# Optimization experiments

Measured on AMD Instinct MI355X. Metric: run time of the kernel, lower is better.

The kernel has to match this reference:

```python
import jax, jax.numpy as jnp
import numpy as np

N = 2048   # query length
M = 2048   # key length
B = 2      # batch
D = 1024   # model dim (d_x_q = d_x_kv = d_out)
H = 16     # heads
DQK = D // H
DV = D // H
OFFSET = 0


def setup_inputs() -> dict:
    key = jax.random.key(0)
    k1, k2, k3, k4, k5, k6 = jax.random.split(key, 6)
    return {
        "x_q": jax.random.normal(k1, (N, B, D), dtype=jnp.float32),
        "x_kv": jax.random.normal(k2, (M, B, D), dtype=jnp.float32),
        "to_q": jax.random.normal(k3, (H, DQK, D), dtype=jnp.float32),
        "to_kv": jax.random.normal(k4, (H, DQK + DV, D), dtype=jnp.float32),
        "for_pos_enc": jax.random.normal(k5, (H, DQK, D), dtype=jnp.float32),
        "to_o": jax.random.normal(k6, (D, H, DV), dtype=jnp.float32),
    }


def _pos_enc(for_pos_enc, n, m, offset, d_x_kv):
    # relative distances i - j + offset, range [offset-(m-1), offset+(n-1)]
    dmin = offset - (m - 1)
    dmax = offset + (n - 1)
    r = jnp.arange(dmin, dmax + 1, dtype=jnp.float32)            # [R]
    inv_freq = 1.0 / (10000.0 ** (jnp.arange(0.0, d_x_kv, 2.0, dtype=jnp.float32) / d_x_kv))
    phases = r[:, None] * inv_freq[None, :]                       # [R, d/2]
    sincos = jnp.concatenate([jnp.sin(phases), jnp.cos(phases)], axis=-1)  # [R, d]
    table = jnp.einsum('hdb,rb->rhd', for_pos_enc, sincos)       # [R, H, DQK]
    dists = jnp.arange(n)[:, None] - jnp.arange(m)[None, :] + offset
    return table[dists - dmin]                                    # [n, m, H, DQK]


def reference(x_q, x_kv, to_q, to_kv, for_pos_enc, to_o):
    d_qk = to_q.shape[1]
    q = jnp.einsum('hdb,nzb->nzhd', to_q, x_q)     # [N,B,H,DQK]
    kv = jnp.einsum('hdb,mzb->mzhd', to_kv, x_kv)  # [M,B,H,DQK+DV]
    k = kv[..., :d_qk]
    v = kv[..., d_qk:]
    n, m = x_q.shape[0], x_kv.shape[0]

    pos_enc = _pos_enc(for_pos_enc, n, m, OFFSET, x_kv.shape[-1])

    content_logits = jnp.einsum('nzhd,mzhd->nmzh', q, k)          # [N,M,B,H]
    position_logits = jnp.einsum('nzhd,nmhd->nmzh', q, pos_enc)   # [N,M,B,H]
    logits = content_logits + position_logits

    # causal mask: True above diagonal shifted by 1+offset
    mask = jnp.triu(jnp.ones((n, m), dtype=bool), 1 + OFFSET)
    logits = jnp.where(mask[:, :, None, None], -jnp.inf, logits)

    weights = jax.nn.softmax(logits, axis=1)
    attn = jnp.einsum('nmzh,mzhd->nzhd', weights, v)              # [N,B,H,DV]
    out = jnp.einsum('dhb,nzhb->nzd', to_o, attn)                 # [N,B,D]
    return out
```

## Files before the change

### kernel.cpp

```cpp
#include <hip/hip_runtime.h>
#include <math.h>

#define NQ 2048
#define MKV 2048
#define BZ 2
#define DM 1024
#define NH 16
#define DH 64
#define RTAB 4095
#define R0TAB 1984
#define MTAB (RTAB - R0TAB)

typedef __bf16 bf16x8 __attribute__((ext_vector_type(8)));
typedef float f32x4 __attribute__((ext_vector_type(4)));

__device__ inline unsigned short f2bf(float x) {
  union { float f; unsigned u; } v; v.f = x;
  unsigned r = (v.u + 0x7FFFu + ((v.u >> 16) & 1u)) >> 16;
  return (unsigned short)r;
}
__device__ inline float bf2f(unsigned short h) {
  union { unsigned u; float f; } v; v.u = ((unsigned)h) << 16; return v.f;
}

#define SWZ(r, b) ((b) ^ (((r) & 7) << 4))
#define VSWZ(dv, m) \
  ((dv) * 128 + (((((m) >> 3) ^ ((dv) & 7) ^ (((dv) >> 3) & 7)) << 4)) + ((m) & 7) * 2)

__device__ inline void gload_lds16(const void* g, void* l) {
  __builtin_amdgcn_global_load_lds((const __attribute__((address_space(1))) void*)g,
                                   (__attribute__((address_space(3))) void*)l, 16, 0, 0);
}

__global__ __launch_bounds__(256) void prep_kernel(
    const float* __restrict__ i0, unsigned short* __restrict__ h0, unsigned short* __restrict__ l0, int n0,
    const float* __restrict__ i1, unsigned short* __restrict__ h1, unsigned short* __restrict__ l1, int n1,
    const float* __restrict__ i2, unsigned short* __restrict__ h2, unsigned short* __restrict__ l2, int n2,
    const float* __restrict__ i3, unsigned short* __restrict__ h3, unsigned short* __restrict__ l3, int n3,
    const float* __restrict__ i4, unsigned short* __restrict__ h4, unsigned short* __restrict__ l4, int n4_,
    const float* __restrict__ i5, unsigned short* __restrict__ h5, unsigned short* __restrict__ l5, int n5,
    unsigned short* __restrict__ schi, unsigned short* __restrict__ sclo) {
  if (blockIdx.y == 6) {
    for (int idx = blockIdx.x * 256 + threadIdx.x; idx < MTAB * DM; idx += gridDim.x * 256) {
      int r = idx / DM;
      int b = idx - r * DM;
      int i = (b < DM / 2) ? b : (b - DM / 2);
      double fr = exp((double)i * (-9.210340371976184 / 512.0));
      float rr = (float)(R0TAB + r - (MKV - 1));
      float ph = rr * (float)fr;
      float val = (b < DM / 2) ? sinf(ph) : cosf(ph);
      unsigned short hb = f2bf(val);
      schi[idx] = hb;
      sclo[idx] = f2bf(val - bf2f(hb));
    }
    return;
  }
  const float* in; unsigned short* hp; unsigned short* lp; int n4;
  switch (blockIdx.y) {
    case 0: in = i0; hp = h0; lp = l0; n4 = n0; break;
    case 1: in = i1; hp = h1; lp = l1; n4 = n1; break;
    case 2: in = i2; hp = h2; lp = l2; n4 = n2; break;
    case 3: in = i3; hp = h3; lp = l3; n4 = n3; break;
    case 4: in = i4; hp = h4; lp = l4; n4 = n4_; break;
    default: in = i5; hp = h5; lp = l5; n4 = n5; break;
  }
  for (int i = blockIdx.x * 256 + threadIdx.x; i < n4; i += gridDim.x * 256) {
    float4 v = ((const float4*)in)[i];
    float f[4] = {v.x, v.y, v.z, v.w};
    ushort4 hq, lq;
    unsigned short* hh = (unsigned short*)&hq;
    unsigned short* ll = (unsigned short*)&lq;
#pragma unroll
    for (int e = 0; e < 4; ++e) {
      unsigned short hb = f2bf(f[e]);
      hh[e] = hb;
      ll[e] = f2bf(f[e] - bf2f(hb));
    }
    ((ushort4*)hp)[i] = hq;
    ((ushort4*)lp)[i] = lq;
  }
}

template <int SPLIT_OUT>
__device__ __forceinline__ void gemm_body(
    const unsigned short* __restrict__ Ahi, const unsigned short* __restrict__ Alo,
    const unsigned short* __restrict__ Bhi, const unsigned short* __restrict__ Blo,
    float* __restrict__ Cf, unsigned short* __restrict__ Chi, unsigned short* __restrict__ Clo,
    int M, int N, int row0, int col0, char* lds) {
  const int K = 1024;
  char* sAh = lds;
  char* sAl = lds + 16384;
  char* sBh = lds + 32768;
  char* sBl = lds + 49152;
  const int t = threadIdx.x;
  const int w = t >> 6;
  const int lane = t & 63;
  const int lo = lane & 15;
  const int hi = lane >> 4;
  const int wm = w >> 1, wn = w & 1;

  f32x4 acc[4][4];
#pragma unroll
  for (int a = 0; a < 4; ++a)
#pragma unroll
    for (int b = 0; b < 4; ++b) acc[a][b] = (f32x4){0.f, 0.f, 0.f, 0.f};

  for (int k0 = 0; k0 < K; k0 += 64) {
#pragma unroll
    for (int i = 0; i < 4; ++i) {
      int L = i * 4096 + t * 16;
      int r = L >> 7;
      int c16 = (L >> 4) & 7;
      int g16 = c16 ^ (r & 7);
      int ra = row0 + r;
      if (ra >= M) ra = M - 1;
      int rb = col0 + r;
      const char* gah = (const char*)(Ahi + (size_t)ra * K + k0) + g16 * 16;
      const char* gal = (const char*)(Alo + (size_t)ra * K + k0) + g16 * 16;
      const char* gbh = (const char*)(Bhi + (size_t)rb * K + k0) + g16 * 16;
      const char* gbl = (const char*)(Blo + (size_t)rb * K + k0) + g16 * 16;
      gload_lds16(gah, sAh + L);
      gload_lds16(gal, sAl + L);
      gload_lds16(gbh, sBh + L);
      gload_lds16(gbl, sBl + L);
    }
    __syncthreads();
#pragma unroll
    for (int ks = 0; ks < 2; ++ks) {
      bf16x8 ah[4], al[4], bh[4], bl[4];
#pragma unroll
      for (int f = 0; f < 4; ++f) {
        int rA = wm * 64 + 16 * f + lo;
        int offA = rA * 128 + (((4 * ks + hi) ^ (rA & 7)) << 4);
        ah[f] = *(const bf16x8*)(sAh + offA);
        al[f] = *(const bf16x8*)(sAl + offA);
        int rB = wn * 64 + 16 * f + lo;
        int offB = rB * 128 + (((4 * ks + hi) ^ (rB & 7)) << 4);
        bh[f] = *(const bf16x8*)(sBh + offB);
        bl[f] = *(const bf16x8*)(sBl + offB);
      }
#pragma unroll
      for (int fm = 0; fm < 4; ++fm)
#pragma unroll
        for (int fn = 0; fn < 4; ++fn) {
          acc[fm][fn] = __builtin_amdgcn_mfma_f32_16x16x32_bf16(ah[fm], bh[fn], acc[fm][fn], 0, 0, 0);
          acc[fm][fn] = __builtin_amdgcn_mfma_f32_16x16x32_bf16(ah[fm], bl[fn], acc[fm][fn], 0, 0, 0);
          acc[fm][fn] = __builtin_amdgcn_mfma_f32_16x16x32_bf16(al[fm], bh[fn], acc[fm][fn], 0, 0, 0);
        }
    }
    __syncthreads();
  }
#pragma unroll
  for (int fm = 0; fm < 4; ++fm)
#pragma unroll
    for (int qq = 0; qq < 4; ++qq) {
      int row = row0 + wm * 64 + 16 * fm + 4 * hi + qq;
      if (row < M) {
#pragma unroll
        for (int fn = 0; fn < 4; ++fn) {
          int col = col0 + wn * 64 + 16 * fn + lo;
          float v = acc[fm][fn][qq];
          if (SPLIT_OUT) {
            unsigned short hb = f2bf(v);
            Chi[(size_t)row * N + col] = hb;
            Clo[(size_t)row * N + col] = f2bf(v - bf2f(hb));
          } else {
            Cf[(size_t)row * N + col] = v;
          }
        }
      }
    }
}

__global__ __launch_bounds__(256, 2) void gemm3_kernel(
    const unsigned short* __restrict__ xqh, const unsigned short* __restrict__ xql,
    const unsigned short* __restrict__ tqh, const unsigned short* __restrict__ tql,
    unsigned short* __restrict__ qh, unsigned short* __restrict__ ql,
    const unsigned short* __restrict__ xkh, const unsigned short* __restrict__ xkl,
    const unsigned short* __restrict__ tkh, const unsigned short* __restrict__ tkl,
    unsigned short* __restrict__ kvh, unsigned short* __restrict__ kvl,
    const unsigned short* __restrict__ sch, const unsigned short* __restrict__ scl,
    const unsigned short* __restrict__ fph, const unsigned short* __restrict__ fpl,
    unsigned short* __restrict__ tbh, unsigned short* __restrict__ tbl) {
  __shared__ char lds[65536];
  int bx = blockIdx.x;
  if (bx < 256) {
    int gx = bx & 7, gy = bx >> 3;
    gemm_body<1>(xqh, xql, tqh, tql, nullptr, qh, ql, 4096, 1024, gy * 128, gx * 128, lds);
  } else if (bx < 768) {
    bx -= 256;
    int gx = bx & 15, gy = bx >> 4;
    gemm_body<1>(xkh, xkl, tkh, tkl, nullptr, kvh, kvl, 4096, 2048, gy * 128, gx * 128, lds);
  } else {
    bx -= 768;
    int gx = bx & 7, gy = bx >> 3;
    gemm_body<1>(sch, scl, fph, fpl, nullptr, tbh, tbl, MTAB, 1024, gy * 128, gx * 128, lds);
  }
}

__global__ __launch_bounds__(256, 2) void gemm_out_kernel(
    const unsigned short* __restrict__ Ahi, const unsigned short* __restrict__ Alo,
    const unsigned short* __restrict__ Bhi, const unsigned short* __restrict__ Blo,
    float* __restrict__ Cf) {
  __shared__ char lds[65536];
  gemm_body<0>(Ahi, Alo, Bhi, Blo, Cf, nullptr, nullptr, 4096, 1024,
               blockIdx.y * 128, blockIdx.x * 128, lds);
}

union U8 { uint4 q; unsigned short u[8]; };

__global__ __launch_bounds__(256, 2) void attn_kernel(
    const unsigned short* __restrict__ qhi, const unsigned short* __restrict__ qlo,
    const unsigned short* __restrict__ kvhi, const unsigned short* __restrict__ kvlo,
    const unsigned short* __restrict__ tabhi, const unsigned short* __restrict__ tablo,
    unsigned short* __restrict__ ohi, unsigned short* __restrict__ olo) {
  __shared__ __align__(16) char sKhi[8192];
  __shared__ __align__(16) char sKlo[8192];
  __shared__ __align__(16) char sT[32768];
  __shared__ __align__(16) char sVT[8192];
  __shared__ __align__(16) char sP[8192];

  const int t = threadIdx.x;
  const int w = t >> 6;
  const int lane = t & 63;
  const int lo = lane & 15;
  const int hi = lane >> 4;

  for (int rep = 0; rep < 2; ++rep) {
    const int item = rep == 0 ? (1023 - (int)blockIdx.x) : (int)blockIdx.x;
    const int qb = item >> 5;
    const int z = (item >> 4) & 1;
    const int h = item & 15;
    const int n0 = qb * 64;

    bf16x8 qh[2], ql[2];
    {
      size_t qoff = (size_t)((n0 + 16 * w + lo) * BZ + z) * DM + h * DH;
#pragma unroll
      for (int ks = 0; ks < 2; ++ks) {
        qh[ks] = *(const bf16x8*)(qhi + qoff + 32 * ks + 8 * hi);
        ql[ks] = *(const bf16x8*)(qlo + qoff + 32 * ks + 8 * hi);
      }
    }

    f32x4 accO[4];
#pragma unroll
    for (int f = 0; f < 4; ++f) accO[f] = (f32x4){0.f, 0.f, 0.f, 0.f};
    float mi[4], li[4];
#pragma unroll
    for (int qq = 0; qq < 4; ++qq) { mi[qq] = -1e30f; li[qq] = 0.f; }

    uint4 pVh[2];
#pragma unroll
    for (int it = 0; it < 2; ++it) {
      int f = it * 256 + t;
      int j = f >> 3;
      int d8 = (f & 7) << 3;
      size_t gb = (size_t)((0 + j) * BZ + z) * (NH * 2 * DH) + h * (2 * DH);
      pVh[it] = *(const uint4*)(kvhi + gb + DH + d8);
    }

    for (int mt = 0; mt <= qb; ++mt) {
      const int m0 = mt * 64;
      const int Wb = n0 - m0 + R0TAB;
      __syncthreads();

#pragma unroll
      for (int it = 0; it < 2; ++it) {
        int f = it * 256 + t;
        int j = f >> 3;
        int c = f & 7;
        int gsw = (c ^ (j & 7)) << 3;
        size_t gb = (size_t)((m0 + j) * BZ + z) * (NH * 2 * DH) + h * (2 * DH);
        gload_lds16(kvhi + gb + gsw, sKhi + f * 16);
        gload_lds16(kvlo + gb + gsw, sKlo + f * 16);
      }
      if (mt == 0) {
#pragma unroll
        for (int it = 0; it < 4; ++it) {
          int f = it * 256 + t;
          int rr = f >> 3;
          int c = f & 7;
          int g = Wb + rr;
          int gc = g < RTAB ? g : (RTAB - 1);
          int slot = g & 127;
          int gsw = (c ^ (g & 7)) << 3;
          size_t gb = (size_t)gc * DM + h * DH;
          gload_lds16(tabhi + gb + gsw, sT + slot * 128 + c * 16);
          gload_lds16(tablo + gb + gsw, sT + 16384 + slot * 128 + c * 16);
        }
      } else {
#pragma unroll
        for (int it = 0; it < 2; ++it) {
          int f = it * 256 + t;
          int rr = f >> 3;
          int c = f & 7;
          int g = Wb + rr;
          int slot = g & 127;
          int gsw = (c ^ (g & 7)) << 3;
          size_t gb = (size_t)g * DM + h * DH;
          gload_lds16(tabhi + gb + gsw, sT + slot * 128 + c * 16);
          gload_lds16(tablo + gb + gsw, sT + 16384 + slot * 128 + c * 16);
        }
      }

#pragma unroll
      for (int it = 0; it < 2; ++it) {
        int f = it * 256 + t;
        int j = f >> 3;
        int d8 = (f & 7) << 3;
        U8 vh;
        vh.q = pVh[it];
#pragma unroll
        for (int e = 0; e < 8; ++e) {
          int dv = d8 + e;
          *(unsigned short*)(sVT + VSWZ(dv, j)) = vh.u[e];
        }
      }
      if (mt < qb) {
        const int m0n = (mt + 1) * 64;
#pragma unroll
        for (int it = 0; it < 2; ++it) {
          int f = it * 256 + t;
          int j = f >> 3;
          int d8 = (f & 7) << 3;
          size_t gb = (size_t)((m0n + j) * BZ + z) * (NH * 2 * DH) + h * (2 * DH);
          pVh[it] = *(const uint4*)(kvhi + gb + DH + d8);
        }
      }
      __syncthreads();

      f32x4 accS[4], accPL[5];
#pragma unroll
      for (int f = 0; f < 4; ++f) accS[f] = (f32x4){0.f, 0.f, 0.f, 0.f};
#pragma unroll
      for (int f = 0; f < 5; ++f) accPL[f] = (f32x4){0.f, 0.f, 0.f, 0.f};
#pragma unroll
      for (int ks = 0; ks < 2; ++ks) {
#pragma unroll
        for (int fm = 0; fm < 4; ++fm) {
          int rb = SWZ(lo, (16 * fm + lo) * 128 + (32 * ks + 8 * hi) * 2);
          bf16x8 kh = *(const bf16x8*)(sKhi + rb);
          bf16x8 kl = *(const bf16x8*)(sKlo + rb);
          accS[fm] = __builtin_amdgcn_mfma_f32_16x16x32_bf16(qh[ks], kh, accS[fm], 0, 0, 0);
          accS[fm] = __builtin_amdgcn_mfma_f32_16x16x32_bf16(qh[ks], kl, accS[fm], 0, 0, 0);
          accS[fm] = __builtin_amdgcn_mfma_f32_16x16x32_bf16(ql[ks], kh, accS[fm], 0, 0, 0);
        }
#pragma unroll
        for (int fr = 0; fr < 5; ++fr) {
          int g = Wb + 16 * (w + fr) + lo;
          int rb = (g & 127) * 128 + (((4 * ks + hi) ^ (g & 7)) << 4);
          bf16x8 th = *(const bf16x8*)(sT + rb);
          bf16x8 tl = *(const bf16x8*)(sT + 16384 + rb);
          accPL[fr] = __builtin_amdgcn_mfma_f32_16x16x32_bf16(qh[ks], th, accPL[fr], 0, 0, 0);
          accPL[fr] = __builtin_amdgcn_mfma_f32_16x16x32_bf16(qh[ks], tl, accPL[fr], 0, 0, 0);
          accPL[fr] = __builtin_amdgcn_mfma_f32_16x16x32_bf16(ql[ks], th, accPL[fr], 0, 0, 0);
        }
      }

#pragma unroll
      for (int fm = 0; fm < 4; ++fm)
#pragma unroll
        for (int qq = 0; qq < 4; ++qq) {
          int rn = 4 * hi + qq + 63 - 16 * fm - lo;
          float va = __shfl(accPL[3 - fm][qq], rn & 15, 16);
          float vb = __shfl(accPL[4 - fm][qq], rn & 15, 16);
          accS[fm][qq] += (rn >> 4) == (3 - fm) ? va : vb;
        }

      if (mt == qb) {
#pragma unroll
        for (int fm = 0; fm < 4; ++fm)
#pragma unroll
          for (int qq = 0; qq < 4; ++qq)
            if (16 * fm + lo > 16 * w + 4 * hi + qq) accS[fm][qq] = -1e30f;
      }

#pragma unroll
      for (int qq = 0; qq < 4; ++qq) {
        float pm = fmaxf(fmaxf(accS[0][qq], accS[1][qq]), fmaxf(accS[2][qq], accS[3][qq]));
        pm = fmaxf(pm, __shfl_xor(pm, 1));
        pm = fmaxf(pm, __shfl_xor(pm, 2));
        pm = fmaxf(pm, __shfl_xor(pm, 4));
        pm = fmaxf(pm, __shfl_xor(pm, 8));
        float mn = fmaxf(mi[qq], pm);
        float a = __expf(mi[qq] - mn);
        mi[qq] = mn;
        float rs = 0.f;
#pragma unroll
        for (int fm = 0; fm < 4; ++fm) {
          float p = __expf(accS[fm][qq] - mn);
          accS[fm][qq] = p;
          rs += p;
        }
        rs += __shfl_xor(rs, 1);
        rs += __shfl_xor(rs, 2);
        rs += __shfl_xor(rs, 4);
        rs += __shfl_xor(rs, 8);
        li[qq] = li[qq] * a + rs;
#pragma unroll
        for (int f = 0; f < 4; ++f) accO[f][qq] *= a;
      }

#pragma unroll
      for (int fm = 0; fm < 4; ++fm)
#pragma unroll
        for (int qq = 0; qq < 4; ++qq) {
          int row = 16 * w + 4 * hi + qq;
          *(unsigned short*)(sP + SWZ(4 * hi + qq, row * 128 + (16 * fm + lo) * 2)) =
              f2bf(accS[fm][qq]);
        }

#pragma unroll
      for (int ks = 0; ks < 2; ++ks) {
        int ab = SWZ(lo, (16 * w + lo) * 128 + (32 * ks + 8 * hi) * 2);
        bf16x8 pa = *(const bf16x8*)(sP + ab);
#pragma unroll
        for (int fv = 0; fv < 4; ++fv) {
          int dv = 16 * fv + lo;
          int vb = dv * 128 + ((((4 * ks + hi) ^ (dv & 7) ^ ((dv >> 3) & 7))) << 4);
          bf16x8 vv = *(const bf16x8*)(sVT + vb);
          accO[fv] = __builtin_amdgcn_mfma_f32_16x16x32_bf16(pa, vv, accO[fv], 0, 0, 0);
        }
      }
    }

#pragma unroll
    for (int qq = 0; qq < 4; ++qq) {
      float inv = 1.0f / li[qq];
      int n = n0 + 16 * w + 4 * hi + qq;
#pragma unroll
      for (int fv = 0; fv < 4; ++fv) {
        size_t idx = (size_t)(n * BZ + z) * DM + h * DH + 16 * fv + lo;
        float v = accO[fv][qq] * inv;
        unsigned short hb = f2bf(v);
        ohi[idx] = hb;
        olo[idx] = f2bf(v - bf2f(hb));
      }
    }
  }
}

extern "C" void kernel_launch(void* const* d_in, const int* in_sizes, int n_in,
                              void* d_out, int out_size, void* d_ws, size_t ws_size,
                              hipStream_t stream) {
  const float* x_q   = (const float*)d_in[0];
  const float* x_kv  = (const float*)d_in[1];
  const float* to_q  = (const float*)d_in[2];
  const float* to_kv = (const float*)d_in[3];
  const float* fpe   = (const float*)d_in[4];
  const float* to_o  = (const float*)d_in[5];
  float* out = (float*)d_out;

  char* W = (char*)d_ws;
  size_t o = 0;
  auto alloc = [&](size_t bytes) { char* p = W + o; o += (bytes + 255) & ~(size_t)255; return p; };
  typedef unsigned short us;
  us* q_hi  = (us*)alloc((size_t)4096 * 1024 * 2);
  us* q_lo  = (us*)alloc((size_t)4096 * 1024 * 2);
  us* kv_hi = (us*)alloc((size_t)4096 * 2048 * 2);
  us* kv_lo = (us*)alloc((size_t)4096 * 2048 * 2);
  us* tab_hi = (us*)alloc((size_t)RTAB * 1024 * 2);
  us* tab_lo = (us*)alloc((size_t)RTAB * 1024 * 2);
  us* xq_hi = (us*)alloc((size_t)4096 * 1024 * 2);
  us* xq_lo = (us*)alloc((size_t)4096 * 1024 * 2);
  us* xkv_hi = (us*)alloc((size_t)4096 * 1024 * 2);
  us* xkv_lo = (us*)alloc((size_t)4096 * 1024 * 2);
  us* tq_hi  = (us*)alloc((size_t)1024 * 1024 * 2);
  us* tq_lo  = (us*)alloc((size_t)1024 * 1024 * 2);
  us* tkv_hi = (us*)alloc((size_t)2048 * 1024 * 2);
  us* tkv_lo = (us*)alloc((size_t)2048 * 1024 * 2);
  us* to_hi  = (us*)alloc((size_t)1024 * 1024 * 2);
  us* to_lo  = (us*)alloc((size_t)1024 * 1024 * 2);
  us* fpe_hi = (us*)alloc((size_t)1024 * 1024 * 2);
  us* fpe_lo = (us*)alloc((size_t)1024 * 1024 * 2);
  us* sc_hi  = (us*)alloc((size_t)MTAB * 1024 * 2);
  us* sc_lo  = (us*)alloc((size_t)MTAB * 1024 * 2);

  prep_kernel<<<dim3(4096, 7), 256, 0, stream>>>(
      x_q,   xq_hi,  xq_lo,  4096 * 1024 / 4,
      x_kv,  xkv_hi, xkv_lo, 4096 * 1024 / 4,
      to_q,  tq_hi,  tq_lo,  1024 * 1024 / 4,
      to_kv, tkv_hi, tkv_lo, 2048 * 1024 / 4,
      to_o,  to_hi,  to_lo,  1024 * 1024 / 4,
      fpe,   fpe_hi, fpe_lo, 1024 * 1024 / 4,
      sc_hi, sc_lo);

  gemm3_kernel<<<dim3(904), 256, 0, stream>>>(
      xq_hi, xq_lo, tq_hi, tq_lo, q_hi, q_lo,
      xkv_hi, xkv_lo, tkv_hi, tkv_lo, kv_hi, kv_lo,
      sc_hi, sc_lo, fpe_hi, fpe_lo,
      tab_hi + (size_t)R0TAB * 1024, tab_lo + (size_t)R0TAB * 1024);

  us* at_hi = xkv_hi;
  us* at_lo = xkv_lo;
  attn_kernel<<<dim3(512), 256, 0, stream>>>(q_hi, q_lo, kv_hi, kv_lo,
                                             tab_hi, tab_lo, at_hi, at_lo);
  gemm_out_kernel<<<dim3(8, 32), 256, 0, stream>>>(at_hi, at_lo, to_hi, to_lo, out);
}
```

Measured before the change: 267.7 us.

## Pre-scale Q by log2e for exp2 softmax, load K-lo directly to registers

The Q projection output is scaled by log2(e) in the GEMM epilogue, so the softmax can use exp2f directly instead of __expf, which multiplies internally. The low-part K tile is no longer staged through LDS; each lane loads its fragment straight from global memory into registers, which frees 8 KB of LDS and removes those LDS writes and reads. The f2bf helper now uses the native __bf16 conversion instead of manual rounding bit arithmetic. The risk is that the direct global loads for K-lo are uncoalesced and their latency is exposed before the MFMA loop, and scaling Q also scales the position logits, which stays consistent only because both use the same Q.

```diff
diff --git a/kernel.cpp b/kernel.cpp
--- a/kernel.cpp
+++ b/kernel.cpp
@@ -10,14 +10,14 @@
 #define RTAB 4095
 #define R0TAB 1984
 #define MTAB (RTAB - R0TAB)
+#define LOG2E 1.44269504088896340736f
 
 typedef __bf16 bf16x8 __attribute__((ext_vector_type(8)));
 typedef float f32x4 __attribute__((ext_vector_type(4)));
 
 __device__ inline unsigned short f2bf(float x) {
-  union { float f; unsigned u; } v; v.f = x;
-  unsigned r = (v.u + 0x7FFFu + ((v.u >> 16) & 1u)) >> 16;
-  return (unsigned short)r;
+  __bf16 b = (__bf16)x;
+  union { __bf16 b; unsigned short u; } v; v.b = b; return v.u;
 }
 __device__ inline float bf2f(unsigned short h) {
   union { unsigned u; float f; } v; v.u = ((unsigned)h) << 16; return v.f;
@@ -86,7 +86,7 @@
     const unsigned short* __restrict__ Ahi, const unsigned short* __restrict__ Alo,
     const unsigned short* __restrict__ Bhi, const unsigned short* __restrict__ Blo,
     float* __restrict__ Cf, unsigned short* __restrict__ Chi, unsigned short* __restrict__ Clo,
-    int M, int N, int row0, int col0, char* lds) {
+    int M, int N, int row0, int col0, char* lds, float cscale) {
   const int K = 1024;
   char* sAh = lds;
   char* sAl = lds + 16384;
@@ -159,7 +159,7 @@
 #pragma unroll
         for (int fn = 0; fn < 4; ++fn) {
           int col = col0 + wn * 64 + 16 * fn + lo;
-          float v = acc[fm][fn][qq];
+          float v = acc[fm][fn][qq] * cscale;
           if (SPLIT_OUT) {
             unsigned short hb = f2bf(v);
             Chi[(size_t)row * N + col] = hb;
@@ -186,15 +186,15 @@
   int bx = blockIdx.x;
   if (bx < 256) {
     int gx = bx & 7, gy = bx >> 3;
-    gemm_body<1>(xqh, xql, tqh, tql, nullptr, qh, ql, 4096, 1024, gy * 128, gx * 128, lds);
+    gemm_body<1>(xqh, xql, tqh, tql, nullptr, qh, ql, 4096, 1024, gy * 128, gx * 128, lds, LOG2E);
   } else if (bx < 768) {
     bx -= 256;
     int gx = bx & 15, gy = bx >> 4;
-    gemm_body<1>(xkh, xkl, tkh, tkl, nullptr, kvh, kvl, 4096, 2048, gy * 128, gx * 128, lds);
+    gemm_body<1>(xkh, xkl, tkh, tkl, nullptr, kvh, kvl, 4096, 2048, gy * 128, gx * 128, lds, 1.0f);
   } else {
     bx -= 768;
     int gx = bx & 7, gy = bx >> 3;
-    gemm_body<1>(sch, scl, fph, fpl, nullptr, tbh, tbl, MTAB, 1024, gy * 128, gx * 128, lds);
+    gemm_body<1>(sch, scl, fph, fpl, nullptr, tbh, tbl, MTAB, 1024, gy * 128, gx * 128, lds, 1.0f);
   }
 }
 
@@ -204,7 +204,7 @@
     float* __restrict__ Cf) {
   __shared__ char lds[65536];
   gemm_body<0>(Ahi, Alo, Bhi, Blo, Cf, nullptr, nullptr, 4096, 1024,
-               blockIdx.y * 128, blockIdx.x * 128, lds);
+               blockIdx.y * 128, blockIdx.x * 128, lds, 1.0f);
 }
 
 union U8 { uint4 q; unsigned short u[8]; };
@@ -215,7 +215,6 @@
     const unsigned short* __restrict__ tabhi, const unsigned short* __restrict__ tablo,
     unsigned short* __restrict__ ohi, unsigned short* __restrict__ olo) {
   __shared__ __align__(16) char sKhi[8192];
-  __shared__ __align__(16) char sKlo[8192];
   __shared__ __align__(16) char sT[32768];
   __shared__ __align__(16) char sVT[8192];
   __shared__ __align__(16) char sP[8192];
@@ -273,7 +272,6 @@
         int gsw = (c ^ (j & 7)) << 3;
         size_t gb = (size_t)((m0 + j) * BZ + z) * (NH * 2 * DH) + h * (2 * DH);
         gload_lds16(kvhi + gb + gsw, sKhi + f * 16);
-        gload_lds16(kvlo + gb + gsw, sKlo + f * 16);
       }
       if (mt == 0) {
 #pragma unroll
@@ -304,6 +302,15 @@
         }
       }
 
+      bf16x8 klf[2][4];
+#pragma unroll
+      for (int ks = 0; ks < 2; ++ks)
+#pragma unroll
+        for (int fm = 0; fm < 4; ++fm)
+          klf[ks][fm] = *(const bf16x8*)(kvlo +
+              (size_t)((m0 + 16 * fm + lo) * BZ + z) * (NH * 2 * DH) + h * (2 * DH) +
+              32 * ks + 8 * hi);
+
 #pragma unroll
       for (int it = 0; it < 2; ++it) {
         int f = it * 256 + t;
@@ -341,9 +348,8 @@
         for (int fm = 0; fm < 4; ++fm) {
           int rb = SWZ(lo, (16 * fm + lo) * 128 + (32 * ks + 8 * hi) * 2);
           bf16x8 kh = *(const bf16x8*)(sKhi + rb);
-          bf16x8 kl = *(const bf16x8*)(sKlo + rb);
           accS[fm] = __builtin_amdgcn_mfma_f32_16x16x32_bf16(qh[ks], kh, accS[fm], 0, 0, 0);
-          accS[fm] = __builtin_amdgcn_mfma_f32_16x16x32_bf16(qh[ks], kl, accS[fm], 0, 0, 0);
+          accS[fm] = __builtin_amdgcn_mfma_f32_16x16x32_bf16(qh[ks], klf[ks][fm], accS[fm], 0, 0, 0);
           accS[fm] = __builtin_amdgcn_mfma_f32_16x16x32_bf16(ql[ks], kh, accS[fm], 0, 0, 0);
         }
 #pragma unroll
@@ -384,12 +390,12 @@
         pm = fmaxf(pm, __shfl_xor(pm, 4));
         pm = fmaxf(pm, __shfl_xor(pm, 8));
         float mn = fmaxf(mi[qq], pm);
-        float a = __expf(mi[qq] - mn);
+        float a = exp2f(mi[qq] - mn);
         mi[qq] = mn;
         float rs = 0.f;
 #pragma unroll
         for (int fm = 0; fm < 4; ++fm) {
-          float p = __expf(accS[fm][qq] - mn);
+          float p = exp2f(accS[fm][qq] - mn);
           accS[fm][qq] = p;
           rs += p;
         }
```

Result: slower. 295.8 us (+10.5%).
